# Performance work log

Hardware: AMD Instinct MI355X
Metric: run time of the kernel (lower is better)

## Reference

```python
import jax, jax.numpy as jnp
import numpy as np

N_WAY = 5
N_SHOT = 25
N_SUPPORT = N_WAY * N_SHOT  # 125
N_QUERY = 2048
D = 8192
C_REG = 0.1        # default C_reg of MetaOptNetHead_SVM_CS
MAX_ITER = 20      # default maxIter of QPFunction
SIGMA = 0.1        # centering parameter of the interior-point iteration


def setup_inputs() -> dict:
    key = jax.random.key(0)
    k1, k2, k3 = jax.random.split(key, 3)
    query = jax.random.normal(k1, (N_QUERY, D), dtype=jnp.float32)
    support = jax.random.normal(k2, (N_SUPPORT, D), dtype=jnp.float32)
    support_labels = jax.random.randint(k3, (N_SUPPORT,), 0, N_WAY, dtype=jnp.int32)
    scale = jnp.ones((1,), dtype=jnp.float32)  # nn.Parameter([1.0])
    return {
        "query": query,
        "support": support,
        "support_labels": support_labels,
        "n_way": N_WAY,
        "n_shot": N_SHOT,
        "scale": scale,
    }


def _solve_qp(G, e, h, A, b):
    """Solve min_z 0.5 z^T G z + e^T z  s.t.  z <= h (C = I),  A z = b.

    Primal-dual infeasible-start interior-point method with MAX_ITER fixed
    Newton steps (the jax analogue of qpth's QPFunction(maxIter=20)).
    Shapes: G (B,n,n), e (B,n), h (B,n), A (B,p,n), b (B,p).
    """
    B, n = e.shape
    p = b.shape[1]
    m = n  # C = I -> one inequality per variable
    At = jnp.swapaxes(A, 1, 2)                      # (B,n,p)
    zero_pp = jnp.zeros((B, p, p), dtype=G.dtype)
    A_row = jnp.concatenate([A, zero_pp], axis=2)   # (B,p,n+p), constant

    z = jnp.zeros_like(e)
    s = jnp.ones_like(h)
    lam = jnp.ones_like(h)
    nu = jnp.zeros_like(b)

    def frac_to_boundary(x, dx):
        # largest alpha in (0,1] keeping x + alpha*dx > 0
        ratio = jnp.where(dx < 0, -x / jnp.where(dx < 0, dx, -1.0), jnp.inf)
        return jnp.min(ratio, axis=1)

    def step(carry, _):
        z, s, lam, nu = carry
        Gz = jnp.einsum('bij,bj->bi', G, z)
        r1 = Gz + e + lam + jnp.einsum('bpi,bp->bi', A, nu)   # dual residual (C^T lam = lam)
        r2 = z + s - h                                         # primal ineq residual
        r4 = jnp.einsum('bpi,bi->bp', A, z) - b                # primal eq residual
        mu = SIGMA * jnp.sum(s * lam, axis=1, keepdims=True) / m
        r3 = lam * s - mu                                      # perturbed complementarity
        # Reduced KKT system: (G + diag(lam/s)) dz + A^T dnu = rhs1 ; A dz = -r4
        H = G + jax.vmap(jnp.diag)(lam / s)                    # (B,n,n)
        rhs1 = -(r1 + (lam * r2 - r3) / s)                     # (B,n)
        K = jnp.concatenate(
            [jnp.concatenate([H, At], axis=2), A_row], axis=1)  # (B,n+p,n+p)
        rhs = jnp.concatenate([rhs1, -r4], axis=1)             # (B,n+p)
        sol = jnp.linalg.solve(K, rhs[..., None])[..., 0]
        dz, dnu = sol[:, :n], sol[:, n:]
        ds = -r2 - dz
        dlam = (-r3 - lam * ds) / s
        alpha = jnp.minimum(
            1.0, 0.99 * jnp.minimum(frac_to_boundary(s, ds),
                                    frac_to_boundary(lam, dlam)))[:, None]
        return (z + alpha * dz, s + alpha * ds,
                lam + alpha * dlam, nu + alpha * dnu), None

    (z, s, lam, nu), _ = jax.lax.scan(step, (z, s, lam, nu), None, length=MAX_ITER)
    return z


def _svm_cs_head(query, support, support_labels, n_way):
    support_b = support[None]            # (1, ns, d) -- head unsqueezes batch dim
    query_b = query[None]                # (1, nq, d)
    B, ns, _ = support_b.shape
    f32 = jnp.float32

    # Gram matrix of support, then kron with I_{n_way} (batched_kronecker == jnp.kron)
    K = jnp.einsum('bnd,bmd->bnm', support_b, support_b)            # (B,ns,ns)
    eye_w = jnp.eye(n_way, dtype=f32)
    G = jax.vmap(lambda k: jnp.kron(k, eye_w))(K)                    # (B,ns*nw,ns*nw)
    G = G + jnp.eye(n_way * ns, dtype=f32)[None]

    y1h = jax.nn.one_hot(support_labels, n_way, dtype=f32).reshape(B, ns * n_way)
    e = -y1h
    h = C_REG * y1h
    A = jnp.kron(jnp.eye(ns, dtype=f32), jnp.ones((1, n_way), f32))[None]  # (1,ns,ns*nw)
    b = jnp.zeros((B, ns), f32)

    qp_sol = _solve_qp(G, e, h, A, b)                                # (B, ns*nw)

    compat = jnp.einsum('bnd,bqd->bnq', support_b, query_b)          # (B,ns,nq)
    qp3 = qp_sol.reshape(B, ns, n_way)
    # logits[b,q,w] = sum_s qp3[b,s,w] * compat[b,s,q]
    logits = jnp.einsum('bsw,bsq->bqw', qp3, compat)                 # (B,nq,nw)
    num_sv = jnp.sum(jnp.any(qp3 > 0.001, axis=2))                   # support-vector count
    return logits, num_sv


def reference(query, support, support_labels, n_way, n_shot, scale):
    logits, num_sv = _svm_cs_head(query, support, support_labels, n_way)
    return scale * logits, num_sv
```

## Files before the change

kernel.cpp:

```cpp
#include <hip/hip_runtime.h>

#define NS   125
#define NW   5
#define NQ   2048
#define DD   8192
#define CREG 0.1f
#define PGD_ITERS 10

#define OFF_PART  0
#define OFF_K     1000000
#define OFF_FLAGS 1015632
#define OFF_QP3   1016000
#define OFF_W     1017000

#define NPART     64
#define QPW_BLKS  129

__global__ __launch_bounds__(256, 2) void gram192(const float* __restrict__ support,
                                                  float* __restrict__ part,
                                                  unsigned int* __restrict__ flags) {
    __shared__ __align__(16) float As[64][132];
    __shared__ __align__(16) float Bs[64][132];
    const int tid = threadIdx.x;
    if (blockIdx.x == 0 && tid == 0) { flags[0] = 0u; flags[1] = 0u; }
    const int qsel = blockIdx.x % 3;
    const int c    = blockIdx.x / 3;
    const int qy = (qsel == 2) ? 1 : 0;
    const int qz = (qsel == 0) ? 0 : 1;
    const int d0 = c * 128;
    const int sy0 = qy * 64, sz0 = qz * 64;

#pragma unroll
    for (int it = 0; it < 8; ++it) {
        int idx = it * 256 + tid;
        int sl = idx >> 5, d4 = idx & 31;
        int sa = sy0 + sl, sb = sz0 + sl;
        float4 va = (sa < NS) ? *(const float4*)&support[(size_t)sa * DD + d0 + d4 * 4]
                              : make_float4(0.f, 0.f, 0.f, 0.f);
        float4 vb = (sb < NS) ? *(const float4*)&support[(size_t)sb * DD + d0 + d4 * 4]
                              : make_float4(0.f, 0.f, 0.f, 0.f);
        *(float4*)&As[sl][d4 * 4] = va;
        *(float4*)&Bs[sl][d4 * 4] = vb;
    }
    __syncthreads();

    const int tx = tid & 15, ty = tid >> 4;
    float acc[4][4];
#pragma unroll
    for (int i = 0; i < 4; i++)
#pragma unroll
        for (int j = 0; j < 4; j++) acc[i][j] = 0.f;

#pragma unroll 4
    for (int d4 = 0; d4 < 32; ++d4) {
        float4 a4[4], b4[4];
#pragma unroll
        for (int i = 0; i < 4; i++) a4[i] = *(const float4*)&As[tx + 16 * i][d4 * 4];
#pragma unroll
        for (int j = 0; j < 4; j++) b4[j] = *(const float4*)&Bs[ty + 16 * j][d4 * 4];
#pragma unroll
        for (int i = 0; i < 4; i++)
#pragma unroll
            for (int j = 0; j < 4; j++)
                acc[i][j] += a4[i].x * b4[j].x + a4[i].y * b4[j].y
                           + a4[i].z * b4[j].z + a4[i].w * b4[j].w;
    }

    float* dst = part + (size_t)c * (NS * NS);
#pragma unroll
    for (int i = 0; i < 4; i++) {
        int gi = sy0 + tx + 16 * i;
        if (gi >= NS) continue;
#pragma unroll
        for (int j = 0; j < 4; j++) {
            int gj = sz0 + ty + 16 * j;
            if (gj < NS) dst[gi * NS + gj] = acc[i][j];
        }
    }
}

__global__ __launch_bounds__(256) void qpw(const float* __restrict__ part,
                                           const int* __restrict__ labels,
                                           const float* __restrict__ support,
                                           float* __restrict__ Kg,
                                           unsigned int* __restrict__ flags,
                                           float* __restrict__ qp3,
                                           float* __restrict__ W,
                                           float* __restrict__ outNumSv) {
    __shared__ __align__(16) float smem[9920];
    __shared__ float rsx[2];
    __shared__ int   svc;
    const int tid = threadIdx.x;
    const int bid = blockIdx.x;

    for (int t = bid * 256 + tid; t < NS * NS; t += QPW_BLKS * 256) {
        int i = t / NS, j = t - i * NS;
        int src = (i >= 64 && j < 64) ? (j * NS + i) : t;
        float s = 0.f;
#pragma unroll 8
        for (int c = 0; c < NPART; ++c) s += part[(size_t)c * (NS * NS) + src];
        Kg[t] = s;
    }
    __syncthreads();
    if (tid == 0)
        __hip_atomic_fetch_add(&flags[0], 1u, __ATOMIC_RELEASE, __HIP_MEMORY_SCOPE_AGENT);

    if (bid == 0) {
        if (tid == 0) {
            while (__hip_atomic_load(&flags[0], __ATOMIC_RELAXED, __HIP_MEMORY_SCOPE_AGENT) < (unsigned)QPW_BLKS)
                __builtin_amdgcn_s_sleep(8);
        }
        __syncthreads();
        (void)__hip_atomic_load(&flags[0], __ATOMIC_ACQUIRE, __HIP_MEMORY_SCOPE_AGENT);

        float* red2 = smem;
        float* zsw  = smem + 6400;
        const int w    = tid >> 6;
        const int lane = tid & 63;
        const int c0   = w * 32;
        const int r0 = lane, r1 = lane + 64;
        float kr0[32], kr1[32];
#pragma unroll
        for (int j = 0; j < 32; ++j) {
            const int col = c0 + j;
            const bool cv = (col < NS);
            kr0[j] = cv ? Kg[col * NS + r0] : 0.f;
            kr1[j] = (cv && r1 < NS) ? Kg[col * NS + r1] : 0.f;
        }
        for (int idx = tid; idx < 2 * 4 * NW * 32; idx += 256) zsw[idx] = 0.f;
        if (tid == 0) svc = 0;
        float rsum0 = 0.f, rsum1 = 0.f;
#pragma unroll
        for (int j = 0; j < 32; ++j) { rsum0 += fabsf(kr0[j]); rsum1 += fabsf(kr1[j]); }
        red2[r0 * 25 + w * 5] = rsum0;
        red2[r1 * 25 + w * 5] = rsum1;
        __syncthreads();
        const int prw = w * 64 + lane;
        if (w < 2) {
            const float* rr = &red2[prw * 25];
            float t = (prw < NS) ? rr[0] + rr[5] + rr[10] + rr[15] : 0.f;
#pragma unroll
            for (int off = 32; off; off >>= 1) t = fmaxf(t, __shfl_xor(t, off));
            if (lane == 0) rsx[w] = t;
        }
        __syncthreads();
        const float eta = 1.9f / (fmaxf(rsx[0], rsx[1]) + 1.0f);
        const int pr  = c0 + lane;
        const bool act = (lane < 32) && (pr < NS);
        const int lab = act ? labels[pr] : 0;
        float z[NW] = {0.f, 0.f, 0.f, 0.f, 0.f};

        for (int it = 0; it < PGD_ITERS; ++it) {
            const int p = it & 1, n = p ^ 1;
            float acc0[NW] = {0.f, 0.f, 0.f, 0.f, 0.f};
            float acc1[NW] = {0.f, 0.f, 0.f, 0.f, 0.f};
            const float* zb = zsw + p * 640 + w * 160;
#pragma unroll
            for (int c = 0; c < 8; ++c) {
                float4 z0 = *(const float4*)&zb[0 * 32 + 4 * c];
                float4 z1 = *(const float4*)&zb[1 * 32 + 4 * c];
                float4 z2 = *(const float4*)&zb[2 * 32 + 4 * c];
                float4 z3 = *(const float4*)&zb[3 * 32 + 4 * c];
                float4 z4 = *(const float4*)&zb[4 * 32 + 4 * c];
                const float k00 = kr0[4*c], k01 = kr0[4*c+1], k02 = kr0[4*c+2], k03 = kr0[4*c+3];
                const float k10 = kr1[4*c], k11 = kr1[4*c+1], k12 = kr1[4*c+2], k13 = kr1[4*c+3];
                acc0[0] += k00*z0.x + k01*z0.y + k02*z0.z + k03*z0.w;
                acc0[1] += k00*z1.x + k01*z1.y + k02*z1.z + k03*z1.w;
                acc0[2] += k00*z2.x + k01*z2.y + k02*z2.z + k03*z2.w;
                acc0[3] += k00*z3.x + k01*z3.y + k02*z3.z + k03*z3.w;
                acc0[4] += k00*z4.x + k01*z4.y + k02*z4.z + k03*z4.w;
                acc1[0] += k10*z0.x + k11*z0.y + k12*z0.z + k13*z0.w;
                acc1[1] += k10*z1.x + k11*z1.y + k12*z1.z + k13*z1.w;
                acc1[2] += k10*z2.x + k11*z2.y + k12*z2.z + k13*z2.w;
                acc1[3] += k10*z3.x + k11*z3.y + k12*z3.z + k13*z3.w;
                acc1[4] += k10*z4.x + k11*z4.y + k12*z4.z + k13*z4.w;
            }
            {
                float* b0 = &red2[p * 3200 + r0 * 25 + w * 5];
                b0[0] = acc0[0]; b0[1] = acc0[1]; b0[2] = acc0[2]; b0[3] = acc0[3]; b0[4] = acc0[4];
                float* b1 = &red2[p * 3200 + r1 * 25 + w * 5];
                b1[0] = acc1[0]; b1[1] = acc1[1]; b1[2] = acc1[2]; b1[3] = acc1[3]; b1[4] = acc1[4];
            }
            __syncthreads();
            if (act) {
                const float* rr = &red2[p * 3200 + pr * 25];
                float v[NW], h[NW];
#pragma unroll
                for (int a = 0; a < NW; a++) {
                    float kz = rr[a] + rr[5 + a] + rr[10 + a] + rr[15 + a];
                    float g = kz + z[a] - ((a == lab) ? 1.f : 0.f);
                    v[a] = z[a] - eta * g;
                    h[a] = (a == lab) ? CREG : 0.f;
                }
                float tau = fmaxf(fmaxf(fmaxf(v[0], v[1]), fmaxf(v[2], v[3])), v[4]);
#pragma unroll
                for (int nn = 0; nn < 7; ++nn) {
                    float g = 0.f, nf = 0.f;
#pragma unroll
                    for (int a = 0; a < NW; a++) {
                        float d = v[a] - tau;
                        bool fr = (d <= h[a]);
                        g += fr ? d : h[a];
                        nf += fr ? 1.f : 0.f;
                    }
                    tau += g / nf;
                }
#pragma unroll
                for (int a = 0; a < NW; a++) {
                    z[a] = fminf(v[a] - tau, h[a]);
                    zsw[n * 640 + w * 160 + a * 32 + lane] = z[a];
                }
            }
        }

        if (act) {
            float m = fmaxf(fmaxf(fmaxf(z[0], z[1]), fmaxf(z[2], z[3])), z[4]);
            if (m > 0.001f) atomicAdd(&svc, 1);
#pragma unroll
            for (int a = 0; a < NW; a++) qp3[pr * NW + a] = z[a];
        }
        __syncthreads();
        if (tid == 0) {
            *outNumSv = (float)svc;
            __hip_atomic_fetch_add(&flags[1], 1u, __ATOMIC_RELEASE, __HIP_MEMORY_SCOPE_AGENT);
        }
    } else {
        float* sup = smem;
        float* q3  = smem + 8000;
        float* red = smem + 8640;
        const int dbase = (bid - 1) * 64;
        for (int idx = tid; idx < NS * 64; idx += 256) {
            int s = idx >> 6, dc = idx & 63;
            sup[idx] = support[(size_t)s * DD + dbase + dc];
        }
        if (tid == 0) {
            while (__hip_atomic_load(&flags[1], __ATOMIC_RELAXED, __HIP_MEMORY_SCOPE_AGENT) < 1u)
                __builtin_amdgcn_s_sleep(16);
        }
        __syncthreads();
        (void)__hip_atomic_load(&flags[1], __ATOMIC_ACQUIRE, __HIP_MEMORY_SCOPE_AGENT);
        for (int i = tid; i < NS * NW; i += 256) q3[i] = qp3[i];
        __syncthreads();
        const int ld = tid & 63;
        const int sq = tid >> 6;
        const int s0 = sq * 32;
        const int s1 = (sq == 3) ? NS : (s0 + 32);
        float acc[NW] = {0.f, 0.f, 0.f, 0.f, 0.f};
#pragma unroll 4
        for (int s = s0; s < s1; ++s) {
            float sv = sup[s * 64 + ld];
#pragma unroll
            for (int a = 0; a < NW; a++) acc[a] += sv * q3[s * NW + a];
        }
        float* rr = &red[tid * NW];
#pragma unroll
        for (int a = 0; a < NW; a++) rr[a] = acc[a];
        __syncthreads();
        if (sq == 0) {
#pragma unroll
            for (int a = 0; a < NW; a++) {
                float s = red[(0 * 64 + ld) * NW + a] + red[(1 * 64 + ld) * NW + a]
                        + red[(2 * 64 + ld) * NW + a] + red[(3 * 64 + ld) * NW + a];
                W[(size_t)a * DD + dbase + ld] = s;
            }
        }
    }
}

__global__ __launch_bounds__(256) void logits8(const float* __restrict__ query,
                                               const float* __restrict__ W,
                                               const float* __restrict__ scale,
                                               float* __restrict__ out) {
    __shared__ float red[4][8][NW];
    const int tid = threadIdx.x;
    const int wave = tid >> 6, lane = tid & 63;
    const int q0 = blockIdx.x * 8;
    const int v0 = wave * 512;
    const float4* W4 = (const float4*)W;
    const float4* q4 = (const float4*)query;
    const float sc = scale[0];

    float acc[8][NW];
#pragma unroll
    for (int k = 0; k < 8; k++)
#pragma unroll
        for (int a = 0; a < NW; a++) acc[k][a] = 0.f;

    for (int it = 0; it < 8; ++it) {
        const int dv = v0 + it * 64 + lane;
        float4 qv[8];
#pragma unroll
        for (int k = 0; k < 8; k++) qv[k] = q4[(size_t)(q0 + k) * (DD / 4) + dv];
#pragma unroll
        for (int a = 0; a < NW; a++) {
            float4 wv = W4[a * (DD / 4) + dv];
#pragma unroll
            for (int k = 0; k < 8; k++)
                acc[k][a] += qv[k].x * wv.x + qv[k].y * wv.y
                           + qv[k].z * wv.z + qv[k].w * wv.w;
        }
    }
#pragma unroll
    for (int off = 32; off; off >>= 1) {
#pragma unroll
        for (int k = 0; k < 8; k++)
#pragma unroll
            for (int a = 0; a < NW; a++) acc[k][a] += __shfl_xor(acc[k][a], off);
    }
    if (lane == 0) {
#pragma unroll
        for (int k = 0; k < 8; k++)
#pragma unroll
            for (int a = 0; a < NW; a++) red[wave][k][a] = acc[k][a];
    }
    __syncthreads();
    if (tid < 8 * NW) {
        const int ql = tid / NW, a = tid % NW;
        float s = red[0][ql][a] + red[1][ql][a] + red[2][ql][a] + red[3][ql][a];
        out[(q0 + ql) * NW + a] = sc * s;
    }
}

extern "C" void kernel_launch(void* const* d_in, const int* in_sizes, int n_in,
                              void* d_out, int out_size, void* d_ws, size_t ws_size,
                              hipStream_t stream) {
    const float* query   = (const float*)d_in[0];
    const float* support = (const float*)d_in[1];
    const int*   labels  = (const int*)d_in[2];
    const float* scale   = (const float*)d_in[5];
    float* out = (float*)d_out;
    float* ws  = (float*)d_ws;

    float* part          = ws + OFF_PART;
    float* Kg            = ws + OFF_K;
    unsigned int* flags  = (unsigned int*)(ws + OFF_FLAGS);
    float* qp3           = ws + OFF_QP3;
    float* W             = ws + OFF_W;

    hipLaunchKernelGGL(gram192, dim3(192), dim3(256), 0, stream, support, part, flags);
    hipLaunchKernelGGL(qpw, dim3(QPW_BLKS), dim3(256), 0, stream,
                       part, labels, support, Kg, flags, qp3, W, out + NQ * NW);
    hipLaunchKernelGGL(logits8, dim3(NQ / 8), dim3(256), 0, stream, query, W, scale, out);
}
```

Measured before the change: 175.5 us.

## Broadcast PGD iterate via readlane, use table reciprocal, widen logits blocks

The PGD loop in the QP block now broadcasts the z iterate across lanes with readlane instead of writing and reading a double-buffered shared-memory array, which removes LDS traffic from each iteration. The division in the tau Newton update is replaced with a select over the reciprocals of 1 to 5. The logits kernel moves to 512-thread blocks, so each wave covers half as much of D and the cross-wave reduction sums 8 partials. The readlane broadcast assumes each 32-column slice of z sits in the same wave's lanes, which matches the current column mapping.

New measurement: 164.2 us. 1.07x faster.

```diff
diff --git a/kernel.cpp b/kernel.cpp
--- a/kernel.cpp
+++ b/kernel.cpp
@@ -114,7 +114,6 @@
         (void)__hip_atomic_load(&flags[0], __ATOMIC_ACQUIRE, __HIP_MEMORY_SCOPE_AGENT);
 
         float* red2 = smem;
-        float* zsw  = smem + 6400;
         const int w    = tid >> 6;
         const int lane = tid & 63;
         const int c0   = w * 32;
@@ -127,7 +126,6 @@
             kr0[j] = cv ? Kg[col * NS + r0] : 0.f;
             kr1[j] = (cv && r1 < NS) ? Kg[col * NS + r1] : 0.f;
         }
-        for (int idx = tid; idx < 2 * 4 * NW * 32; idx += 256) zsw[idx] = 0.f;
         if (tid == 0) svc = 0;
         float rsum0 = 0.f, rsum1 = 0.f;
 #pragma unroll
@@ -151,29 +149,21 @@
         float z[NW] = {0.f, 0.f, 0.f, 0.f, 0.f};
 
         for (int it = 0; it < PGD_ITERS; ++it) {
-            const int p = it & 1, n = p ^ 1;
+            const int p = it & 1;
             float acc0[NW] = {0.f, 0.f, 0.f, 0.f, 0.f};
             float acc1[NW] = {0.f, 0.f, 0.f, 0.f, 0.f};
-            const float* zb = zsw + p * 640 + w * 160;
-#pragma unroll
-            for (int c = 0; c < 8; ++c) {
-                float4 z0 = *(const float4*)&zb[0 * 32 + 4 * c];
-                float4 z1 = *(const float4*)&zb[1 * 32 + 4 * c];
-                float4 z2 = *(const float4*)&zb[2 * 32 + 4 * c];
-                float4 z3 = *(const float4*)&zb[3 * 32 + 4 * c];
-                float4 z4 = *(const float4*)&zb[4 * 32 + 4 * c];
-                const float k00 = kr0[4*c], k01 = kr0[4*c+1], k02 = kr0[4*c+2], k03 = kr0[4*c+3];
-                const float k10 = kr1[4*c], k11 = kr1[4*c+1], k12 = kr1[4*c+2], k13 = kr1[4*c+3];
-                acc0[0] += k00*z0.x + k01*z0.y + k02*z0.z + k03*z0.w;
-                acc0[1] += k00*z1.x + k01*z1.y + k02*z1.z + k03*z1.w;
-                acc0[2] += k00*z2.x + k01*z2.y + k02*z2.z + k03*z2.w;
-                acc0[3] += k00*z3.x + k01*z3.y + k02*z3.z + k03*z3.w;
-                acc0[4] += k00*z4.x + k01*z4.y + k02*z4.z + k03*z4.w;
-                acc1[0] += k10*z0.x + k11*z0.y + k12*z0.z + k13*z0.w;
-                acc1[1] += k10*z1.x + k11*z1.y + k12*z1.z + k13*z1.w;
-                acc1[2] += k10*z2.x + k11*z2.y + k12*z2.z + k13*z2.w;
-                acc1[3] += k10*z3.x + k11*z3.y + k12*z3.z + k13*z3.w;
-                acc1[4] += k10*z4.x + k11*z4.y + k12*z4.z + k13*z4.w;
+#pragma unroll
+            for (int j = 0; j < 32; ++j) {
+                float zj[NW];
+#pragma unroll
+                for (int a = 0; a < NW; a++)
+                    zj[a] = __uint_as_float(__builtin_amdgcn_readlane(__float_as_uint(z[a]), j));
+                const float k0 = kr0[j], k1 = kr1[j];
+#pragma unroll
+                for (int a = 0; a < NW; a++) {
+                    acc0[a] = fmaf(k0, zj[a], acc0[a]);
+                    acc1[a] = fmaf(k1, zj[a], acc1[a]);
+                }
             }
             {
                 float* b0 = &red2[p * 3200 + r0 * 25 + w * 5];
@@ -203,13 +193,15 @@
                         g += fr ? d : h[a];
                         nf += fr ? 1.f : 0.f;
                     }
-                    tau += g / nf;
+                    float rnf = (nf > 4.5f) ? 0.2f
+                              : (nf > 3.5f) ? 0.25f
+                              : (nf > 2.5f) ? (1.f / 3.f)
+                              : (nf > 1.5f) ? 0.5f : 1.f;
+                    tau += g * rnf;
                 }
 #pragma unroll
-                for (int a = 0; a < NW; a++) {
+                for (int a = 0; a < NW; a++)
                     z[a] = fminf(v[a] - tau, h[a]);
-                    zsw[n * 640 + w * 160 + a * 32 + lane] = z[a];
-                }
             }
         }
 
@@ -267,15 +259,15 @@
     }
 }
 
-__global__ __launch_bounds__(256) void logits8(const float* __restrict__ query,
-                                               const float* __restrict__ W,
-                                               const float* __restrict__ scale,
-                                               float* __restrict__ out) {
-    __shared__ float red[4][8][NW];
+__global__ __launch_bounds__(512) void logits8w(const float* __restrict__ query,
+                                                const float* __restrict__ W,
+                                                const float* __restrict__ scale,
+                                                float* __restrict__ out) {
+    __shared__ float red[8][8][NW];
     const int tid = threadIdx.x;
     const int wave = tid >> 6, lane = tid & 63;
     const int q0 = blockIdx.x * 8;
-    const int v0 = wave * 512;
+    const int v0 = wave * 256;
     const float4* W4 = (const float4*)W;
     const float4* q4 = (const float4*)query;
     const float sc = scale[0];
@@ -286,7 +278,7 @@
 #pragma unroll
         for (int a = 0; a < NW; a++) acc[k][a] = 0.f;
 
-    for (int it = 0; it < 8; ++it) {
+    for (int it = 0; it < 4; ++it) {
         const int dv = v0 + it * 64 + lane;
         float4 qv[8];
 #pragma unroll
@@ -316,7 +308,9 @@
     __syncthreads();
     if (tid < 8 * NW) {
         const int ql = tid / NW, a = tid % NW;
-        float s = red[0][ql][a] + red[1][ql][a] + red[2][ql][a] + red[3][ql][a];
+        float s = 0.f;
+#pragma unroll
+        for (int wv = 0; wv < 8; ++wv) s += red[wv][ql][a];
         out[(q0 + ql) * NW + a] = sc * s;
     }
 }
@@ -340,5 +334,5 @@
     hipLaunchKernelGGL(gram192, dim3(192), dim3(256), 0, stream, support, part, flags);
     hipLaunchKernelGGL(qpw, dim3(QPW_BLKS), dim3(256), 0, stream,
                        part, labels, support, Kg, flags, qp3, W, out + NQ * NW);
-    hipLaunchKernelGGL(logits8, dim3(NQ / 8), dim3(256), 0, stream, query, W, scale, out);
+    hipLaunchKernelGGL(logits8w, dim3(NQ / 8), dim3(512), 0, stream, query, W, scale, out);
 }
```
